# Performance work log

Hardware: AMD Instinct MI355X
Metric: run time of the kernel (lower is better)

## Reference

```python
import jax, jax.numpy as jnp
import numpy as np

ALPHA = 0.7
L_CHAMFER, L_EDGE, L_SMOOTH, L_NORMAL = 1.0, 2.0, 1.0, 0.5
EPS = 1e-8

N, M, P, G, F = 8192, 8192, 8192, 8192, 16384


def _cdist(a, b):
    # Euclidean distance matrix, (N,3) x (M,3) -> (N,M); matches torch.cdist
    d2 = (jnp.sum(a * a, axis=1)[:, None]
          + jnp.sum(b * b, axis=1)[None, :]
          - 2.0 * a @ b.T)
    return jnp.sqrt(jnp.maximum(d2, 0.0))


def _chamfer(a, b):
    d = _cdist(a, b)
    return (d.min(axis=1).mean() + d.min(axis=0).mean()) * 0.5


def _unit(x, key):
    v = jax.random.normal(key, x, dtype=jnp.float32)
    return v / jnp.linalg.norm(v, axis=1, keepdims=True)


def setup_inputs() -> dict:
    key = jax.random.key(0)
    ks = jax.random.split(key, 7)
    return {
        "student_verts": jax.random.normal(ks[0], (N, 3), dtype=jnp.float32),
        "student_normals": _unit((N, 3), ks[1]),
        "teacher_verts": jax.random.normal(ks[2], (M, 3), dtype=jnp.float32),
        "teacher_normals": _unit((M, 3), ks[3]),
        "teacher_points": jax.random.normal(ks[4], (P, 3), dtype=jnp.float32),
        "gt_points": jax.random.normal(ks[5], (G, 3), dtype=jnp.float32),
        "faces": jax.random.randint(ks[6], (F, 3), 0, N, dtype=jnp.int32),
    }


def reference(student_verts, student_normals, teacher_verts, teacher_normals,
              teacher_points, gt_points, faces):
    # --- chamfer losses ---
    loss_teacher = _chamfer(student_verts, teacher_points)
    loss_gt = _chamfer(student_verts, gt_points)
    loss_chamfer = ALPHA * loss_teacher + (1.0 - ALPHA) * loss_gt

    # --- mesh edge loss: mean squared edge length ---
    edges = jnp.concatenate([faces[:, [0, 1]], faces[:, [1, 2]], faces[:, [2, 0]]], axis=0)  # (3F,2)
    ev = student_verts[edges[:, 0]] - student_verts[edges[:, 1]]
    loss_edge = jnp.sum(ev * ev, axis=1).mean()

    # --- uniform laplacian smoothing: mean || mean(nbrs) - v || ---
    nverts = student_verts.shape[0]
    src = jnp.concatenate([edges[:, 0], edges[:, 1]])
    dst = jnp.concatenate([edges[:, 1], edges[:, 0]])
    nbr_sum = jax.ops.segment_sum(student_verts[dst], src, num_segments=nverts)
    deg = jax.ops.segment_sum(jnp.ones_like(src, dtype=jnp.float32), src, num_segments=nverts)
    lap = nbr_sum / jnp.maximum(deg, 1.0)[:, None] - student_verts
    loss_smooth = jnp.linalg.norm(lap, axis=1).mean()
    # replicate norm with safe sqrt for grad stability

    # --- normal loss via nearest teacher vertex ---
    d_tv = _cdist(student_verts, teacher_verts)  # (N,M)
    nearest_idx = jnp.argmin(d_tv, axis=1)
    target_normals = teacher_normals[nearest_idx]  # (N,3)
    num = jnp.sum(student_normals * target_normals, axis=1)
    den = (jnp.maximum(jnp.linalg.norm(student_normals, axis=1), EPS)
           * jnp.maximum(jnp.linalg.norm(target_normals, axis=1), EPS))
    loss_normal = 1.0 - (num / den).mean()

    total = (L_CHAMFER * loss_chamfer + L_EDGE * loss_edge
             + L_SMOOTH * loss_smooth + L_NORMAL * loss_normal)
    return total
```

## Files before the change

### kernel.cpp

```cpp
#include <hip/hip_runtime.h>


#define BLK 256
#define TA  4
#define JC  128

__device__ __forceinline__ float wave_reduce_sum(float v) {
#pragma unroll
  for (int o = 32; o > 0; o >>= 1) v += __shfl_down(v, o, 64);
  return v;
}

__device__ __forceinline__ unsigned flipf(float f) {
  unsigned b = __float_as_uint(f);
  return (b & 0x80000000u) ? ~b : (b | 0x80000000u);
}
__device__ __forceinline__ float unflipf(unsigned u) {
  unsigned b = (u & 0x80000000u) ? (u ^ 0x80000000u) : ~u;
  return __uint_as_float(b);
}

__global__ void init_ws_kernel(unsigned long long* __restrict__ min64, int n64,
                               unsigned* __restrict__ minbits, int nmin,
                               float* __restrict__ zr, int nz) {
  const int stride = gridDim.x * blockDim.x;
  const int t0 = blockIdx.x * blockDim.x + threadIdx.x;
  for (int i = t0; i < n64; i += stride) min64[i] = ~0ull;
  for (int i = t0; i < nmin; i += stride) minbits[i] = 0xFF800000u;
  for (int i = t0; i < nz; i += stride) zr[i] = 0.0f;
}

struct PassDesc {
  const float* A[5];
  const float* B[5];
  void* out[5];
};

__global__ void __launch_bounds__(BLK) pairs_kernel(PassDesc pd, int nRows, int nCols) {
  const int pass = blockIdx.z;
  const float* __restrict__ A = pd.A[pass];
  const float* __restrict__ B = pd.B[pass];
  __shared__ float4 sB[JC];

  const int j0 = blockIdx.y * JC;
  const int t = threadIdx.x;
  if (t < JC && j0 + t < nCols) {
    const int j = j0 + t;
    float bx = B[3 * j], by = B[3 * j + 1], bz = B[3 * j + 2];
    sB[t] = make_float4(bx, by, bz, fmaf(bx, bx, fmaf(by, by, bz * bz)));
  }

  const int rowBase = blockIdx.x * (TA * BLK) + t;
  float nax[TA], nay[TA], naz[TA], m[TA];
#pragma unroll
  for (int k = 0; k < TA; ++k) {
    int r = rowBase + k * BLK;
    int rc = (r < nRows) ? r : 0;
    nax[k] = -2.0f * A[3 * rc + 0];
    nay[k] = -2.0f * A[3 * rc + 1];
    naz[k] = -2.0f * A[3 * rc + 2];
    m[k] = __int_as_float(0x7f800000);
  }
  __syncthreads();

  const int jcnt = min(JC, nCols - j0);

  if (pass < 4) {
#pragma unroll 4
    for (int jj = 0; jj < jcnt; ++jj) {
      float4 b = sB[jj];
#pragma unroll
      for (int k = 0; k < TA; ++k)
        m[k] = fminf(m[k], fmaf(nax[k], b.x, fmaf(nay[k], b.y, fmaf(naz[k], b.z, b.w))));
    }
    unsigned* __restrict__ out = (unsigned*)pd.out[pass];
#pragma unroll
    for (int k = 0; k < TA; ++k) {
      int r = rowBase + k * BLK;
      if (r < nRows) atomicMin(out + r, flipf(m[k]));
    }
  } else {
    int idx[TA];
#pragma unroll
    for (int k = 0; k < TA; ++k) idx[k] = j0;
#pragma unroll 4
    for (int jj = 0; jj < jcnt; ++jj) {
      float4 b = sB[jj];
#pragma unroll
      for (int k = 0; k < TA; ++k) {
        float d = fmaf(nax[k], b.x, fmaf(nay[k], b.y, fmaf(naz[k], b.z, b.w)));
        if (d < m[k]) { m[k] = d; idx[k] = j0 + jj; }
      }
    }
    unsigned long long* __restrict__ out = (unsigned long long*)pd.out[pass];
#pragma unroll
    for (int k = 0; k < TA; ++k) {
      int r = rowBase + k * BLK;
      unsigned long long packed =
          ((unsigned long long)flipf(m[k]) << 32) | (unsigned)idx[k];
      if (r < nRows) atomicMin(out + r, packed);
    }
  }
}

__global__ void edge_kernel(const int* __restrict__ fc, int f,
                            const float* __restrict__ v,
                            float* __restrict__ nbr, float* __restrict__ deg,
                            float* __restrict__ acc) {
  const int e = blockIdx.x * blockDim.x + threadIdx.x;
  const int nE = 3 * f;
  float es = 0.f;
  if (e < nE) {
    int a, b;
    if (e < f) { a = fc[3 * e + 0]; b = fc[3 * e + 1]; }
    else if (e < 2 * f) { int tt = e - f; a = fc[3 * tt + 1]; b = fc[3 * tt + 2]; }
    else { int tt = e - 2 * f; a = fc[3 * tt + 2]; b = fc[3 * tt + 0]; }
    float axv = v[3 * a], ayv = v[3 * a + 1], azv = v[3 * a + 2];
    float bxv = v[3 * b], byv = v[3 * b + 1], bzv = v[3 * b + 2];
    float dx = axv - bxv, dy = ayv - byv, dz = azv - bzv;
    es = fmaf(dx, dx, fmaf(dy, dy, dz * dz));
    atomicAdd(&nbr[3 * a + 0], bxv);
    atomicAdd(&nbr[3 * a + 1], byv);
    atomicAdd(&nbr[3 * a + 2], bzv);
    atomicAdd(&nbr[3 * b + 0], axv);
    atomicAdd(&nbr[3 * b + 1], ayv);
    atomicAdd(&nbr[3 * b + 2], azv);
    atomicAdd(&deg[a], 1.0f);
    atomicAdd(&deg[b], 1.0f);
  }
  es = wave_reduce_sum(es);
  if ((threadIdx.x & 63) == 0) atomicAdd(&acc[4], es);
}

__global__ void post_kernel(const float* __restrict__ sv,
                            const float* __restrict__ sn,
                            const float* __restrict__ tn,
                            const float* __restrict__ tp,
                            const float* __restrict__ gp,
                            const float* __restrict__ nbr,
                            const float* __restrict__ deg,
                            const unsigned* __restrict__ minbase,
                            const unsigned long long* __restrict__ min64,
                            int n, int p, float* __restrict__ acc) {
  const int task = blockIdx.y;
  const int i = blockIdx.x * blockDim.x + threadIdx.x;
  float s = 0.f;
  int accIdx;
  if (task == 0) {
    accIdx = 5;
    if (i < n) {
      float d = fmaxf(deg[i], 1.0f);
      float lx = nbr[3 * i + 0] / d - sv[3 * i + 0];
      float ly = nbr[3 * i + 1] / d - sv[3 * i + 1];
      float lz = nbr[3 * i + 2] / d - sv[3 * i + 2];
      s = sqrtf(fmaf(lx, lx, fmaf(ly, ly, lz * lz)));
    }
  } else if (task == 1) {
    accIdx = 6;
    if (i < n) {
      int idx = (int)(min64[i] & 0xffffffffull);
      float sx = sn[3 * i], sy = sn[3 * i + 1], sz = sn[3 * i + 2];
      float tx = tn[3 * idx], ty = tn[3 * idx + 1], tz = tn[3 * idx + 2];
      float num = fmaf(sx, tx, fmaf(sy, ty, sz * tz));
      float ns = sqrtf(fmaf(sx, sx, fmaf(sy, sy, sz * sz)));
      float nt = sqrtf(fmaf(tx, tx, fmaf(ty, ty, tz * tz)));
      s = num / (fmaxf(ns, 1e-8f) * fmaxf(nt, 1e-8f));
    }
  } else {
    const int seg = task - 2;
    accIdx = seg;
    const float* Aarr = (seg == 1) ? tp : (seg == 3) ? gp : sv;
    const int off = (seg == 0) ? 0 : (seg == 1) ? n : (seg == 2) ? (n + p) : (2 * n + p);
    const int cnt = (seg == 1) ? p : n;
    if (i < cnt) {
      float mval = unflipf(minbase[off + i]);
      float ax = Aarr[3 * i], ay = Aarr[3 * i + 1], az = Aarr[3 * i + 2];
      float aa = fmaf(ax, ax, fmaf(ay, ay, az * az));
      s = sqrtf(fmaxf(mval + aa, 0.0f));
    }
  }
  s = wave_reduce_sum(s);
  if ((threadIdx.x & 63) == 0) atomicAdd(&acc[accIdx], s);
}

__global__ void final_kernel(const float* __restrict__ acc,
                             float* __restrict__ out,
                             int n, int p, int g, int nE) {
  float lt = 0.5f * (acc[0] / (float)n + acc[1] / (float)p);
  float lg = 0.5f * (acc[2] / (float)n + acc[3] / (float)g);
  float chamfer = 0.7f * lt + 0.3f * lg;
  float edge = acc[4] / (float)nE;
  float smooth = acc[5] / (float)n;
  float normal = 1.0f - acc[6] / (float)n;
  out[0] = chamfer + 2.0f * edge + smooth + 0.5f * normal;
}

extern "C" void kernel_launch(void* const* d_in, const int* in_sizes, int n_in,
                              void* d_out, int out_size, void* d_ws, size_t ws_size,
                              hipStream_t stream) {
  const float* sv = (const float*)d_in[0];
  const float* sn = (const float*)d_in[1];
  const float* tv = (const float*)d_in[2];
  const float* tn = (const float*)d_in[3];
  const float* tp = (const float*)d_in[4];
  const float* gp = (const float*)d_in[5];
  const int*   fc = (const int*)d_in[6];
  const int n = in_sizes[0] / 3;
  const int m = in_sizes[2] / 3;
  const int p = in_sizes[4] / 3;
  const int g = in_sizes[5] / 3;
  const int f = in_sizes[6] / 3;

  char* w = (char*)d_ws;
  unsigned long long* min64 = (unsigned long long*)w; w += (size_t)n * 8;
  unsigned* minbase = (unsigned*)w;
  w += (size_t)(n + p + n + g) * 4;
  float* nbr = (float*)w; w += (size_t)n * 3 * 4;
  float* deg = (float*)w; w += (size_t)n * 4;
  float* acc = (float*)w;

  unsigned* minA_tp = minbase;
  unsigned* minB_tp = minA_tp + n;
  unsigned* minA_gt = minB_tp + p;
  unsigned* minB_gt = minA_gt + n;

  const int nmin = n + p + n + g;
  const int nz = n * 3 + n + 8;

  init_ws_kernel<<<128, BLK, 0, stream>>>(min64, n, minbase, nmin, nbr, nz);

  PassDesc pd;
  pd.A[0] = sv; pd.B[0] = tp; pd.out[0] = minA_tp;
  pd.A[1] = tp; pd.B[1] = sv; pd.out[1] = minB_tp;
  pd.A[2] = sv; pd.B[2] = gp; pd.out[2] = minA_gt;
  pd.A[3] = gp; pd.B[3] = sv; pd.out[3] = minB_gt;
  pd.A[4] = sv; pd.B[4] = tv; pd.out[4] = min64;

  dim3 pgrid((n + TA * BLK - 1) / (TA * BLK), (n + JC - 1) / JC, 5);
  pairs_kernel<<<pgrid, BLK, 0, stream>>>(pd, n, n);

  edge_kernel<<<(3 * f + BLK - 1) / BLK, BLK, 0, stream>>>(fc, f, sv, nbr, deg, acc);

  dim3 tgrid((n + BLK - 1) / BLK, 6);
  post_kernel<<<tgrid, BLK, 0, stream>>>(sv, sn, tn, tp, gp, nbr, deg,
                                         minbase, min64, n, p, acc);

  final_kernel<<<1, 1, 0, stream>>>(acc, (float*)d_out, n, p, g, 3 * f);
}
```

Measured before the change: 134.9 us.

## Fuse edge pass into pairwise kernel, pack-math distances, fold final reduction

Merges the edge/Laplacian scatter work into the pairwise min kernel as an extra grid slice, and folds the final scalar combine into the post kernel via a last-block counter. This removes two launches. Enlarges row and column tiles (TA 8, JC 256) and switches the inner loop to SoA shared memory with 2-wide vector FMA/min so packed FP32 instructions can be used. Nearest-index tracking now uses float indices, which are exact for these sizes. The larger tiles raise register pressure and shrink the grid, and padded columns rely on a sentinel weight.

```diff
diff --git a/kernel.cpp b/kernel.cpp
--- a/kernel.cpp
+++ b/kernel.cpp
@@ -1,9 +1,12 @@
 #include <hip/hip_runtime.h>
 
 
+typedef float f32x2 __attribute__((ext_vector_type(2)));
+typedef float f32x4 __attribute__((ext_vector_type(4)));
+
 #define BLK 256
-#define TA  4
-#define JC  128
+#define TA 8
+#define JC 256
 
 __device__ __forceinline__ float wave_reduce_sum(float v) {
 #pragma unroll
@@ -18,6 +21,10 @@
 __device__ __forceinline__ float unflipf(unsigned u) {
   unsigned b = (u & 0x80000000u) ? (u ^ 0x80000000u) : ~u;
   return __uint_as_float(b);
+}
+
+__device__ __forceinline__ f32x2 splat2(float v) {
+  f32x2 r; r.x = v; r.y = v; return r;
 }
 
 __global__ void init_ws_kernel(unsigned long long* __restrict__ min64, int n64,
@@ -30,118 +37,155 @@
   for (int i = t0; i < nz; i += stride) zr[i] = 0.0f;
 }
 
-struct PassDesc {
+struct Desc {
   const float* A[5];
   const float* B[5];
   void* out[5];
+  const int* fc; int f;
+  const float* sv;
+  float* nbr; float* deg; float* acc;
+  int nRows, nCols;
 };
 
-__global__ void __launch_bounds__(BLK) pairs_kernel(PassDesc pd, int nRows, int nCols) {
+__global__ void __launch_bounds__(BLK) mega_kernel(Desc d) {
   const int pass = blockIdx.z;
-  const float* __restrict__ A = pd.A[pass];
-  const float* __restrict__ B = pd.B[pass];
-  __shared__ float4 sB[JC];
-
+  const int t = threadIdx.x;
+
+  if (pass == 5) {
+    const int nE = 3 * d.f;
+    const int bid = blockIdx.y * gridDim.x + blockIdx.x;
+    const int stride = gridDim.x * gridDim.y * BLK;
+    float es = 0.f;
+    for (int e = bid * BLK + t; e < nE; e += stride) {
+      int a, b;
+      if (e < d.f)            { a = d.fc[3 * e + 0];  b = d.fc[3 * e + 1]; }
+      else if (e < 2 * d.f)   { int q = e - d.f;     a = d.fc[3 * q + 1]; b = d.fc[3 * q + 2]; }
+      else                    { int q = e - 2 * d.f; a = d.fc[3 * q + 2]; b = d.fc[3 * q + 0]; }
+      float ax = d.sv[3 * a], ay = d.sv[3 * a + 1], az = d.sv[3 * a + 2];
+      float bx = d.sv[3 * b], by = d.sv[3 * b + 1], bz = d.sv[3 * b + 2];
+      float dx = ax - bx, dy = ay - by, dz = az - bz;
+      es += fmaf(dx, dx, fmaf(dy, dy, dz * dz));
+      atomicAdd(&d.nbr[3 * a + 0], bx);
+      atomicAdd(&d.nbr[3 * a + 1], by);
+      atomicAdd(&d.nbr[3 * a + 2], bz);
+      atomicAdd(&d.nbr[3 * b + 0], ax);
+      atomicAdd(&d.nbr[3 * b + 1], ay);
+      atomicAdd(&d.nbr[3 * b + 2], az);
+      atomicAdd(&d.deg[a], 1.0f);
+      atomicAdd(&d.deg[b], 1.0f);
+    }
+    es = wave_reduce_sum(es);
+    if ((t & 63) == 0) atomicAdd(&d.acc[4], es);
+    return;
+  }
+
+  __shared__ f32x4 sX[JC / 4], sY[JC / 4], sZ[JC / 4], sW[JC / 4];
+  const float* __restrict__ A = d.A[pass];
+  const float* __restrict__ B = d.B[pass];
   const int j0 = blockIdx.y * JC;
-  const int t = threadIdx.x;
-  if (t < JC && j0 + t < nCols) {
-    const int j = j0 + t;
-    float bx = B[3 * j], by = B[3 * j + 1], bz = B[3 * j + 2];
-    sB[t] = make_float4(bx, by, bz, fmaf(bx, bx, fmaf(by, by, bz * bz)));
+  {
+    int j = j0 + t;
+    float bx = 0.f, by = 0.f, bz = 0.f, bw = 1e30f;
+    if (j < d.nCols) {
+      bx = B[3 * j]; by = B[3 * j + 1]; bz = B[3 * j + 2];
+      bw = fmaf(bx, bx, fmaf(by, by, bz * bz));
+    }
+    ((float*)sX)[t] = bx; ((float*)sY)[t] = by;
+    ((float*)sZ)[t] = bz; ((float*)sW)[t] = bw;
   }
 
   const int rowBase = blockIdx.x * (TA * BLK) + t;
-  float nax[TA], nay[TA], naz[TA], m[TA];
+  f32x2 nax[TA], nay[TA], naz[TA], m2[TA];
 #pragma unroll
   for (int k = 0; k < TA; ++k) {
     int r = rowBase + k * BLK;
-    int rc = (r < nRows) ? r : 0;
-    nax[k] = -2.0f * A[3 * rc + 0];
-    nay[k] = -2.0f * A[3 * rc + 1];
-    naz[k] = -2.0f * A[3 * rc + 2];
-    m[k] = __int_as_float(0x7f800000);
+    int rc = (r < d.nRows) ? r : 0;
+    nax[k] = splat2(-2.0f * A[3 * rc + 0]);
+    nay[k] = splat2(-2.0f * A[3 * rc + 1]);
+    naz[k] = splat2(-2.0f * A[3 * rc + 2]);
+    m2[k] = splat2(1e30f);
   }
   __syncthreads();
 
-  const int jcnt = min(JC, nCols - j0);
-
   if (pass < 4) {
-#pragma unroll 4
-    for (int jj = 0; jj < jcnt; ++jj) {
-      float4 b = sB[jj];
-#pragma unroll
-      for (int k = 0; k < TA; ++k)
-        m[k] = fminf(m[k], fmaf(nax[k], b.x, fmaf(nay[k], b.y, fmaf(naz[k], b.z, b.w))));
-    }
-    unsigned* __restrict__ out = (unsigned*)pd.out[pass];
+#pragma unroll 2
+    for (int jg = 0; jg < JC / 4; ++jg) {
+      f32x4 X = sX[jg], Y = sY[jg], Z = sZ[jg], W = sW[jg];
+      f32x2 x01 = X.xy, x23 = X.zw;
+      f32x2 y01 = Y.xy, y23 = Y.zw;
+      f32x2 z01 = Z.xy, z23 = Z.zw;
+      f32x2 w01 = W.xy, w23 = W.zw;
+#pragma unroll
+      for (int k = 0; k < TA; ++k) {
+        f32x2 d01 = __builtin_elementwise_fma(naz[k], z01, w01);
+        d01 = __builtin_elementwise_fma(nay[k], y01, d01);
+        d01 = __builtin_elementwise_fma(nax[k], x01, d01);
+        f32x2 d23 = __builtin_elementwise_fma(naz[k], z23, w23);
+        d23 = __builtin_elementwise_fma(nay[k], y23, d23);
+        d23 = __builtin_elementwise_fma(nax[k], x23, d23);
+        f32x2 dm = __builtin_elementwise_min(d01, d23);
+        m2[k] = __builtin_elementwise_min(m2[k], dm);
+      }
+    }
+    unsigned* __restrict__ out = (unsigned*)d.out[pass];
 #pragma unroll
     for (int k = 0; k < TA; ++k) {
       int r = rowBase + k * BLK;
-      if (r < nRows) atomicMin(out + r, flipf(m[k]));
+      if (r < d.nRows) atomicMin(out + r, flipf(fminf(m2[k].x, m2[k].y)));
     }
   } else {
-    int idx[TA];
-#pragma unroll
-    for (int k = 0; k < TA; ++k) idx[k] = j0;
-#pragma unroll 4
-    for (int jj = 0; jj < jcnt; ++jj) {
-      float4 b = sB[jj];
+    f32x2 id2[TA];
+#pragma unroll
+    for (int k = 0; k < TA; ++k) id2[k] = splat2(0.f);
+#pragma unroll 2
+    for (int jg = 0; jg < JC / 4; ++jg) {
+      f32x4 X = sX[jg], Y = sY[jg], Z = sZ[jg], W = sW[jg];
+      f32x2 x01 = X.xy, x23 = X.zw;
+      f32x2 y01 = Y.xy, y23 = Y.zw;
+      f32x2 z01 = Z.xy, z23 = Z.zw;
+      f32x2 w01 = W.xy, w23 = W.zw;
+      float jb = (float)(j0 + 4 * jg);
+      float j1f = jb + 1.f, j2f = jb + 2.f, j3f = jb + 3.f;
 #pragma unroll
       for (int k = 0; k < TA; ++k) {
-        float d = fmaf(nax[k], b.x, fmaf(nay[k], b.y, fmaf(naz[k], b.z, b.w)));
-        if (d < m[k]) { m[k] = d; idx[k] = j0 + jj; }
+        f32x2 d01 = __builtin_elementwise_fma(naz[k], z01, w01);
+        d01 = __builtin_elementwise_fma(nay[k], y01, d01);
+        d01 = __builtin_elementwise_fma(nax[k], x01, d01);
+        f32x2 d23 = __builtin_elementwise_fma(naz[k], z23, w23);
+        d23 = __builtin_elementwise_fma(nay[k], y23, d23);
+        d23 = __builtin_elementwise_fma(nax[k], x23, d23);
+        bool c0 = d01.x < m2[k].x;
+        m2[k].x = c0 ? d01.x : m2[k].x;  id2[k].x = c0 ? jb  : id2[k].x;
+        bool c1 = d01.y < m2[k].y;
+        m2[k].y = c1 ? d01.y : m2[k].y;  id2[k].y = c1 ? j1f : id2[k].y;
+        bool c2 = d23.x < m2[k].x;
+        m2[k].x = c2 ? d23.x : m2[k].x;  id2[k].x = c2 ? j2f : id2[k].x;
+        bool c3 = d23.y < m2[k].y;
+        m2[k].y = c3 ? d23.y : m2[k].y;  id2[k].y = c3 ? j3f : id2[k].y;
       }
     }
-    unsigned long long* __restrict__ out = (unsigned long long*)pd.out[pass];
+    unsigned long long* __restrict__ out = (unsigned long long*)d.out[4];
 #pragma unroll
     for (int k = 0; k < TA; ++k) {
       int r = rowBase + k * BLK;
-      unsigned long long packed =
-          ((unsigned long long)flipf(m[k]) << 32) | (unsigned)idx[k];
-      if (r < nRows) atomicMin(out + r, packed);
-    }
-  }
-}
-
-__global__ void edge_kernel(const int* __restrict__ fc, int f,
-                            const float* __restrict__ v,
-                            float* __restrict__ nbr, float* __restrict__ deg,
-                            float* __restrict__ acc) {
-  const int e = blockIdx.x * blockDim.x + threadIdx.x;
-  const int nE = 3 * f;
-  float es = 0.f;
-  if (e < nE) {
-    int a, b;
-    if (e < f) { a = fc[3 * e + 0]; b = fc[3 * e + 1]; }
-    else if (e < 2 * f) { int tt = e - f; a = fc[3 * tt + 1]; b = fc[3 * tt + 2]; }
-    else { int tt = e - 2 * f; a = fc[3 * tt + 2]; b = fc[3 * tt + 0]; }
-    float axv = v[3 * a], ayv = v[3 * a + 1], azv = v[3 * a + 2];
-    float bxv = v[3 * b], byv = v[3 * b + 1], bzv = v[3 * b + 2];
-    float dx = axv - bxv, dy = ayv - byv, dz = azv - bzv;
-    es = fmaf(dx, dx, fmaf(dy, dy, dz * dz));
-    atomicAdd(&nbr[3 * a + 0], bxv);
-    atomicAdd(&nbr[3 * a + 1], byv);
-    atomicAdd(&nbr[3 * a + 2], bzv);
-    atomicAdd(&nbr[3 * b + 0], axv);
-    atomicAdd(&nbr[3 * b + 1], ayv);
-    atomicAdd(&nbr[3 * b + 2], azv);
-    atomicAdd(&deg[a], 1.0f);
-    atomicAdd(&deg[b], 1.0f);
-  }
-  es = wave_reduce_sum(es);
-  if ((threadIdx.x & 63) == 0) atomicAdd(&acc[4], es);
-}
-
-__global__ void post_kernel(const float* __restrict__ sv,
-                            const float* __restrict__ sn,
-                            const float* __restrict__ tn,
-                            const float* __restrict__ tp,
-                            const float* __restrict__ gp,
-                            const float* __restrict__ nbr,
-                            const float* __restrict__ deg,
-                            const unsigned* __restrict__ minbase,
-                            const unsigned long long* __restrict__ min64,
-                            int n, int p, float* __restrict__ acc) {
+      unsigned long long pa =
+          ((unsigned long long)flipf(m2[k].x) << 32) | (unsigned)(int)id2[k].x;
+      unsigned long long pb =
+          ((unsigned long long)flipf(m2[k].y) << 32) | (unsigned)(int)id2[k].y;
+      unsigned long long best = pa < pb ? pa : pb;
+      if (r < d.nRows) atomicMin(out + r, best);
+    }
+  }
+}
+
+__global__ void __launch_bounds__(BLK) post_kernel(
+    const float* __restrict__ sv, const float* __restrict__ sn,
+    const float* __restrict__ tn, const float* __restrict__ tp,
+    const float* __restrict__ gp, const float* __restrict__ nbr,
+    const float* __restrict__ deg, const unsigned* __restrict__ minbase,
+    const unsigned long long* __restrict__ min64,
+    int n, int p, int g, int f, float* __restrict__ acc,
+    int* __restrict__ cnt, float* __restrict__ out) {
   const int task = blockIdx.y;
   const int i = blockIdx.x * blockDim.x + threadIdx.x;
   float s = 0.f;
@@ -149,10 +193,10 @@
   if (task == 0) {
     accIdx = 5;
     if (i < n) {
-      float d = fmaxf(deg[i], 1.0f);
-      float lx = nbr[3 * i + 0] / d - sv[3 * i + 0];
-      float ly = nbr[3 * i + 1] / d - sv[3 * i + 1];
-      float lz = nbr[3 * i + 2] / d - sv[3 * i + 2];
+      float dd = fmaxf(deg[i], 1.0f);
+      float lx = nbr[3 * i + 0] / dd - sv[3 * i + 0];
+      float ly = nbr[3 * i + 1] / dd - sv[3 * i + 1];
+      float lz = nbr[3 * i + 2] / dd - sv[3 * i + 2];
       s = sqrtf(fmaf(lx, lx, fmaf(ly, ly, lz * lz)));
     }
   } else if (task == 1) {
@@ -171,8 +215,8 @@
     accIdx = seg;
     const float* Aarr = (seg == 1) ? tp : (seg == 3) ? gp : sv;
     const int off = (seg == 0) ? 0 : (seg == 1) ? n : (seg == 2) ? (n + p) : (2 * n + p);
-    const int cnt = (seg == 1) ? p : n;
-    if (i < cnt) {
+    const int cntN = (seg == 1) ? p : n;
+    if (i < cntN) {
       float mval = unflipf(minbase[off + i]);
       float ax = Aarr[3 * i], ay = Aarr[3 * i + 1], az = Aarr[3 * i + 2];
       float aa = fmaf(ax, ax, fmaf(ay, ay, az * az));
@@ -181,18 +225,25 @@
   }
   s = wave_reduce_sum(s);
   if ((threadIdx.x & 63) == 0) atomicAdd(&acc[accIdx], s);
-}
-
-__global__ void final_kernel(const float* __restrict__ acc,
-                             float* __restrict__ out,
-                             int n, int p, int g, int nE) {
-  float lt = 0.5f * (acc[0] / (float)n + acc[1] / (float)p);
-  float lg = 0.5f * (acc[2] / (float)n + acc[3] / (float)g);
-  float chamfer = 0.7f * lt + 0.3f * lg;
-  float edge = acc[4] / (float)nE;
-  float smooth = acc[5] / (float)n;
-  float normal = 1.0f - acc[6] / (float)n;
-  out[0] = chamfer + 2.0f * edge + smooth + 0.5f * normal;
+
+  __syncthreads();
+  __threadfence();
+  __shared__ int last;
+  if (threadIdx.x == 0)
+    last = (atomicAdd(cnt, 1) == (int)(gridDim.x * gridDim.y) - 1);
+  __syncthreads();
+  if (last && threadIdx.x == 0) {
+    float a[7];
+#pragma unroll
+    for (int q = 0; q < 7; ++q) a[q] = atomicAdd(&acc[q], 0.0f);
+    float lt = 0.5f * (a[0] / (float)n + a[1] / (float)p);
+    float lg = 0.5f * (a[2] / (float)n + a[3] / (float)g);
+    float chamfer = 0.7f * lt + 0.3f * lg;
+    float edge = a[4] / (float)(3 * f);
+    float smooth = a[5] / (float)n;
+    float normal = 1.0f - a[6] / (float)n;
+    out[0] = chamfer + 2.0f * edge + smooth + 0.5f * normal;
+  }
 }
 
 extern "C" void kernel_launch(void* const* d_in, const int* in_sizes, int n_in,
@@ -213,11 +264,11 @@
 
   char* w = (char*)d_ws;
   unsigned long long* min64 = (unsigned long long*)w; w += (size_t)n * 8;
-  unsigned* minbase = (unsigned*)w;
-  w += (size_t)(n + p + n + g) * 4;
+  unsigned* minbase = (unsigned*)w; w += (size_t)(n + p + n + g) * 4;
   float* nbr = (float*)w; w += (size_t)n * 3 * 4;
   float* deg = (float*)w; w += (size_t)n * 4;
-  float* acc = (float*)w;
+  float* acc = (float*)w; w += 8 * 4;
+  int* cnt = (int*)w;
 
   unsigned* minA_tp = minbase;
   unsigned* minB_tp = minA_tp + n;
@@ -225,25 +276,25 @@
   unsigned* minB_gt = minA_gt + n;
 
   const int nmin = n + p + n + g;
-  const int nz = n * 3 + n + 8;
-
-  init_ws_kernel<<<128, BLK, 0, stream>>>(min64, n, minbase, nmin, nbr, nz);
-
-  PassDesc pd;
-  pd.A[0] = sv; pd.B[0] = tp; pd.out[0] = minA_tp;
-  pd.A[1] = tp; pd.B[1] = sv; pd.out[1] = minB_tp;
-  pd.A[2] = sv; pd.B[2] = gp; pd.out[2] = minA_gt;
-  pd.A[3] = gp; pd.B[3] = sv; pd.out[3] = minB_gt;
-  pd.A[4] = sv; pd.B[4] = tv; pd.out[4] = min64;
-
-  dim3 pgrid((n + TA * BLK - 1) / (TA * BLK), (n + JC - 1) / JC, 5);
-  pairs_kernel<<<pgrid, BLK, 0, stream>>>(pd, n, n);
-
-  edge_kernel<<<(3 * f + BLK - 1) / BLK, BLK, 0, stream>>>(fc, f, sv, nbr, deg, acc);
+  const int nz = n * 3 + n + 8 + 1;
+
+  init_ws_kernel<<<64, BLK, 0, stream>>>(min64, n, minbase, nmin, nbr, nz);
+
+  Desc d;
+  d.A[0] = sv; d.B[0] = tp; d.out[0] = minA_tp;
+  d.A[1] = tp; d.B[1] = sv; d.out[1] = minB_tp;
+  d.A[2] = sv; d.B[2] = gp; d.out[2] = minA_gt;
+  d.A[3] = gp; d.B[3] = sv; d.out[3] = minB_gt;
+  d.A[4] = sv; d.B[4] = tv; d.out[4] = min64;
+  d.fc = fc; d.f = f; d.sv = sv;
+  d.nbr = nbr; d.deg = deg; d.acc = acc;
+  d.nRows = n; d.nCols = n;
+
+  dim3 pgrid((n + TA * BLK - 1) / (TA * BLK), (n + JC - 1) / JC, 6);
+  mega_kernel<<<pgrid, BLK, 0, stream>>>(d);
 
   dim3 tgrid((n + BLK - 1) / BLK, 6);
   post_kernel<<<tgrid, BLK, 0, stream>>>(sv, sn, tn, tp, gp, nbr, deg,
-                                         minbase, min64, n, p, acc);
-
-  final_kernel<<<1, 1, 0, stream>>>(acc, (float*)d_out, n, p, g, 3 * f);
-}
+                                         minbase, min64, n, p, g, f,
+                                         acc, cnt, (float*)d_out);
+}
```

Result: faster. 129.2 us (-4.2%).
